# Kernel tuning notes

Measured on AMD Instinct MI355X. Metric: run time of the kernel, lower is better.

The kernel has to match this reference:

```python
import jax, jax.numpy as jnp
import numpy as np

N, E, G = 50000, 1600000, 64
N_SPECIES, D_ATTR, D, N_RBF = 16, 16, 32, 8
CUTOFF = 5.0
SCALE, SHIFT = 1.0, 0.0


def setup_inputs() -> dict:
    key = jax.random.key(0)
    ks = jax.random.split(key, 20)

    def w(k, shape):
        fan_in = shape[-2] if len(shape) > 1 else shape[-1]
        return jax.random.normal(k, shape, dtype=jnp.float32) / np.sqrt(fan_in)

    return {
        "x": jax.random.randint(ks[0], (N, 1), 0, N_SPECIES),
        "pos": 3.0 * jax.random.normal(ks[1], (N, 3), dtype=jnp.float32),
        "edge_index": jax.random.randint(ks[2], (2, E), 0, N),
        "period_vec": 0.1 * jax.random.normal(ks[3], (E, 3), dtype=jnp.float32),
        "batch": jnp.sort(jax.random.randint(ks[4], (N,), 0, G)),
        "W_elem": w(ks[5], (N_SPECIES, D_ATTR)),
        "W0": w(ks[6], (D_ATTR, D)),
        "b0": jnp.zeros((D,), jnp.float32),
        "Wr1": w(ks[7], (3, N_RBF, D)),
        "br1": jnp.zeros((3, D), jnp.float32),
        "Wr2": w(ks[8], (3, D, D)),
        "Wmsg": w(ks[9], (3, D, D)),
        "Wattr": w(ks[10], (3, D_ATTR, D)),
        "Wself": w(ks[11], (3, D, D)),
        "bconv": jnp.zeros((3, D), jnp.float32),
        "wsh": w(ks[12], (3, 4)),
        "Wp1": w(ks[13], (D, 16)),
        "bp1": jnp.zeros((16,), jnp.float32),
        "Wp2": w(ks[14], (16, 1)),
        "bp2": jnp.zeros((1,), jnp.float32),
    }


def reference(x, pos, edge_index, period_vec, batch, W_elem, W0, b0, Wr1, br1,
              Wr2, Wmsg, Wattr, Wself, bconv, wsh, Wp1, bp1, Wp2, bp2):
    src, dst = edge_index[0], edge_index[1]

    # node_attr_layer: species embedding (gather), then first_atom_embed linear
    x_attr = W_elem[x[:, 0]]                              # [N, D_ATTR]
    h = x_attr @ W0 + b0                                  # [N, D]

    # edge_attr_layer: PBC edge vectors, lengths, l<=1 spherical harmonics
    edge_vec = pos[dst] - pos[src] + period_vec           # [E, 3]
    edge_len = jnp.linalg.norm(edge_vec, axis=-1, keepdims=True)  # [E, 1]
    unit = edge_vec / (edge_len + 1e-9)
    edge_sh = jnp.concatenate([jnp.ones_like(edge_len), unit], axis=-1)  # [E, 4]

    # edge_embedding_layer: Gaussian radial basis of edge lengths
    centers = jnp.linspace(0.0, CUTOFF, N_RBF, dtype=pos.dtype)
    gamma = jnp.asarray((N_RBF / CUTOFF) ** 2, pos.dtype)
    rbf = jnp.exp(-gamma * (edge_len - centers) ** 2)     # [E, N_RBF]

    # 3 conv layers: gather -> per-edge transform -> scatter-sum -> node update
    for i in range(3):
        rw = jax.nn.relu(rbf @ Wr1[i] + br1[i]) @ Wr2[i]  # [E, D] radial MLP
        sh_w = edge_sh @ wsh[i]                           # [E] sh mixing
        msg = (h[src] @ Wmsg[i]) * rw * sh_w[:, None]     # [E, D]
        agg = jax.ops.segment_sum(msg, dst, num_segments=N)  # [N, D]
        h = jax.nn.silu(agg + x_attr @ Wattr[i] + h @ Wself[i] + bconv[i])

    # post_conv layers
    h = jax.nn.silu(h @ Wp1 + bp1)                        # [N, 16]
    h = (h @ Wp2 + bp2)[:, 0]                             # [N] (squeeze)

    # scatter-sum pooling over graphs + affine energy scaling
    e = jax.ops.segment_sum(h, batch, num_segments=G)     # [G]
    return (e * SCALE + SHIFT)[:, None]                   # [G, 1]
```

## Files before the change

### kernel.cpp

```cpp
#include <hip/hip_runtime.h>
#include <hip/hip_fp16.h>
#include <math.h>

constexpr int N_NODES  = 50000;
constexpr int N_EDGES  = 1600000;
constexpr int G_GRAPHS = 64;
constexpr int D        = 32;
constexpr int D_ATTR   = 16;
constexpr int N_RBF    = 8;

constexpr int   TBL      = 8192;
constexpr int   TBL_ROWS = TBL + 1;
constexpr float LMAX     = 10.0f;

constexpr int BUCKET = 80;

constexpr int NT     = 64;
constexpr int NTILES = (N_NODES + NT - 1) / NT;
constexpr int TCAP   = 2432;
constexpr int EPB      = 2048;
constexpr int STHREADS = 512;
constexpr int EPV      = EPB / STHREADS;
constexpr int NBLK1    = (N_EDGES + EPB - 1) / EPB;

constexpr int NSLOT = NTILES * NT * BUCKET;

typedef unsigned int  uint4v  __attribute__((ext_vector_type(4)));
typedef unsigned int  uint2v  __attribute__((ext_vector_type(2)));

__device__ __forceinline__ float silu(float x) {
    return x / (1.0f + __expf(-x));
}
__device__ __forceinline__ float h2f_bits(unsigned short u) {
    return __half2float(__ushort_as_half(u));
}
__device__ __forceinline__ __half2 h2u(unsigned v) {
    union { unsigned u; __half2 h; } c; c.u = v; return c.h;
}

__global__ void node_init_kernel(const int* __restrict__ x,
                                 const float* __restrict__ W_elem,
                                 const float* __restrict__ W0,
                                 const float* __restrict__ b0,
                                 const float* __restrict__ Wmsg0,
                                 const float* __restrict__ Wself0,
                                 const float* __restrict__ Wattr,
                                 const float* __restrict__ bconv,
                                 __half* __restrict__ hm0,
                                 float* __restrict__ hs0,
                                 float* __restrict__ xa1,
                                 float* __restrict__ xa2,
                                 float* __restrict__ out) {
    int t = blockIdx.x * blockDim.x + threadIdx.x;
    if (t < G_GRAPHS) out[t] = 0.0f;
    int n = t >> 5, c = t & 31;
    if (n >= N_NODES) return;
    int sp = x[n];
    const float* we = W_elem + sp * D_ATTR;
    float xv = (c < D_ATTR) ? we[c] : 0.0f;
    float acc = b0[c];
#pragma unroll
    for (int a = 0; a < D_ATTR; ++a) acc += we[a] * W0[a * D + c];
    float m = 0.0f, s = 0.0f;
#pragma unroll
    for (int j = 0; j < D; ++j) {
        float hj = __shfl(acc, j, 32);
        m = fmaf(hj, Wmsg0[j * D + c], m);
        s = fmaf(hj, Wself0[j * D + c], s);
    }
    float a0 = bconv[0 * D + c], a1 = bconv[1 * D + c], a2 = bconv[2 * D + c];
#pragma unroll
    for (int j = 0; j < D_ATTR; ++j) {
        float xj = __shfl(xv, j, 32);
        a0 = fmaf(xj, Wattr[0 * D_ATTR * D + j * D + c], a0);
        a1 = fmaf(xj, Wattr[1 * D_ATTR * D + j * D + c], a1);
        a2 = fmaf(xj, Wattr[2 * D_ATTR * D + j * D + c], a2);
    }
    hm0[n * D + c] = __float2half(m);
    hs0[n * D + c] = s + a0;
    xa1[n * D + c] = a1;
    xa2[n * D + c] = a2;
}

__global__ __launch_bounds__(STHREADS) void hist_kernel(const int* __restrict__ eidx,
                                                        int* __restrict__ blk_hist) {
    __shared__ int hist[NTILES];
    int tid = threadIdx.x;
    int e0 = blockIdx.x * EPB;
    for (int i = tid; i < NTILES; i += STHREADS) hist[i] = 0;
    __syncthreads();
#pragma unroll
    for (int i = 0; i < EPV; ++i) {
        int e = e0 + tid + STHREADS * i;
        if (e < N_EDGES) atomicAdd(&hist[eidx[N_EDGES + e] >> 6], 1);
    }
    __syncthreads();
    int* dst = blk_hist + (size_t)blockIdx.x * NTILES;
    for (int t = tid; t < NTILES; t += STHREADS) dst[t] = hist[t];
}

__global__ void scan_kernel(const int* __restrict__ blk_hist,
                            int* __restrict__ blk_base,
                            int* __restrict__ tile_total) {
    int t = blockIdx.x;
    int lane = threadIdx.x;
    int run = 0;
    for (int b0 = 0; b0 < NBLK1; b0 += 64) {
        int b = b0 + lane;
        int v = (b < NBLK1) ? blk_hist[(size_t)b * NTILES + t] : 0;
        int pre = v;
#pragma unroll
        for (int o = 1; o < 64; o <<= 1) {
            int w = __shfl_up(pre, o);
            if (lane >= o) pre += w;
        }
        int excl = pre - v;
        if (b < NBLK1) blk_base[(size_t)b * NTILES + t] = run + excl;
        run += __shfl(pre, 63);
    }
    if (lane == 0) tile_total[t] = run;
}

__global__ __launch_bounds__(STHREADS) void scatter_kernel(const int* __restrict__ eidx,
                                                           const float* __restrict__ pos,
                                                           const float* __restrict__ period,
                                                           const float* __restrict__ wsh,
                                                           const int* __restrict__ blk_base,
                                                           uint4v* __restrict__ bins) {
    __shared__ int hist[NTILES];
    __shared__ int basev[NTILES];
    int tid = threadIdx.x;
    int e0 = blockIdx.x * EPB;
    const int* bb = blk_base + (size_t)blockIdx.x * NTILES;
    for (int i = tid; i < NTILES; i += STHREADS) {
        hist[i] = 0;
        basev[i] = bb[i];
    }
    __syncthreads();

    int   sarr[EPV], darr[EPV];
    float vx[EPV], vy[EPV], vz[EPV];
#pragma unroll
    for (int i = 0; i < EPV; ++i) {
        int e  = e0 + tid + STHREADS * i;
        int ec = (e < N_EDGES) ? e : (N_EDGES - 1);
        int s = eidx[ec];
        int d = eidx[N_EDGES + ec];
        sarr[i] = s;
        darr[i] = d;
        vx[i] = pos[d * 3 + 0] - pos[s * 3 + 0] + period[ec * 3 + 0];
        vy[i] = pos[d * 3 + 1] - pos[s * 3 + 1] + period[ec * 3 + 1];
        vz[i] = pos[d * 3 + 2] - pos[s * 3 + 2] + period[ec * 3 + 2];
    }
    asm volatile("" ::
        "v"(vx[0]), "v"(vx[1]), "v"(vx[2]), "v"(vx[3]),
        "v"(vy[0]), "v"(vy[1]), "v"(vy[2]), "v"(vy[3]),
        "v"(vz[0]), "v"(vz[1]), "v"(vz[2]), "v"(vz[3]),
        "v"(sarr[0]), "v"(sarr[1]), "v"(sarr[2]), "v"(sarr[3]),
        "v"(darr[0]), "v"(darr[1]), "v"(darr[2]), "v"(darr[3]));
#pragma unroll
    for (int i = 0; i < EPV; ++i) {
        int e = e0 + tid + STHREADS * i;
        if (e >= N_EDGES) continue;
        float len = sqrtf(vx[i] * vx[i] + vy[i] * vy[i] + vz[i] * vz[i]);
        float inv = 1.0f / (len + 1e-9f);
        int idx = (int)fminf(len * ((float)TBL / LMAX) + 0.5f, (float)TBL);
        float sw[3];
#pragma unroll
        for (int l = 0; l < 3; ++l)
            sw[l] = wsh[l * 4 + 0] +
                    (vx[i] * wsh[l * 4 + 1] + vy[i] * wsh[l * 4 + 2] + vz[i] * wsh[l * 4 + 3]) * inv;
        int tile = darr[i] >> 6;
        int rank = atomicAdd(&hist[tile], 1);
        int slot = basev[tile] + rank;
        if (slot < TCAP) {
            unsigned u0 = (unsigned)__half_as_ushort(__float2half(sw[0]));
            unsigned u1 = (unsigned)__half_as_ushort(__float2half(sw[1]));
            unsigned u2 = (unsigned)__half_as_ushort(__float2half(sw[2]));
            uint4v r;
            r.x = (unsigned)sarr[i] | ((unsigned)idx << 16);
            r.y = (unsigned)(darr[i] & (NT - 1));
            r.z = u0 | (u1 << 16);
            r.w = u2;
            bins[(size_t)tile * TCAP + slot] = r;
        }
    }
}

__global__ __launch_bounds__(512) void shuffle_kernel(const uint4v* __restrict__ bins,
                                                      const int* __restrict__ tile_total,
                                                      unsigned int* __restrict__ xs,
                                                      unsigned short* __restrict__ swp,
                                                      int* __restrict__ count) {
    __shared__ int lcur[NT];
    int tile = blockIdx.x;
    int tid = threadIdx.x;
    if (tid < NT) lcur[tid] = 0;
    __syncthreads();
    int cnt = tile_total[tile];
    if (cnt > TCAP) cnt = TCAP;
    const uint4v* base = bins + (size_t)tile * TCAP;
    for (int i = tid; i < cnt; i += 512) {
        uint4v r = __builtin_nontemporal_load(base + i);
        int dl = (int)(r.y & 63u);
        int slot = atomicAdd(&lcur[dl], 1);
        if (slot < BUCKET) {
            size_t g = (size_t)(tile * NT + dl) * BUCKET + slot;
            xs[g] = r.x;
            swp[0 * (size_t)NSLOT + g] = (unsigned short)(r.z & 0xFFFFu);
            swp[1 * (size_t)NSLOT + g] = (unsigned short)(r.z >> 16);
            swp[2 * (size_t)NSLOT + g] = (unsigned short)(r.w & 0xFFFFu);
        }
    }
    __syncthreads();
    if (tid < NT) {
        int node = tile * NT + tid;
        if (node < N_NODES) {
            int c = lcur[tid];
            count[node] = c < BUCKET ? c : BUCKET;
        }
    }
}

__global__ void table_kernel(const float* __restrict__ Wr1,
                             const float* __restrict__ br1,
                             const float* __restrict__ Wr2,
                             __half* __restrict__ table) {
    int t = blockIdx.x * blockDim.x + threadIdx.x;
    if (t >= 3 * TBL_ROWS) return;
    int l = t / TBL_ROWS;
    int idx = t % TBL_ROWS;
    float len = (float)idx * (LMAX / (float)TBL);
    const float gamma = (8.0f / 5.0f) * (8.0f / 5.0f);
    float rbf[N_RBF];
#pragma unroll
    for (int k = 0; k < N_RBF; ++k) {
        float dd = len - (float)k * (5.0f / 7.0f);
        rbf[k] = __expf(-gamma * dd * dd);
    }
    float out[D];
#pragma unroll
    for (int c = 0; c < D; ++c) out[c] = 0.0f;
    for (int j = 0; j < D; ++j) {
        float z = br1[l * D + j];
#pragma unroll
        for (int k = 0; k < N_RBF; ++k) z += rbf[k] * Wr1[l * N_RBF * D + k * D + j];
        z = fmaxf(z, 0.0f);
        const float* w2 = Wr2 + l * D * D + j * D;
#pragma unroll
        for (int c = 0; c < D; ++c) out[c] += z * w2[c];
    }
    __half* dst = table + ((size_t)(l * TBL_ROWS + idx)) * D;
#pragma unroll
    for (int c = 0; c < D; ++c) dst[c] = __float2half(out[c]);
}

template <int LAYER, bool NEXT>
__global__ __launch_bounds__(256, 4) void conv_kernel(const __half* __restrict__ hm,
                            const float* __restrict__ hs,
                            const unsigned int* __restrict__ xs,
                            const unsigned short* __restrict__ swp,
                            const int* __restrict__ count,
                            const __half* __restrict__ table,
                            const float* __restrict__ Wmsg_next,
                            const float* __restrict__ Wself_next,
                            const float* __restrict__ xa_next,
                            __half* __restrict__ hm_out,
                            float* __restrict__ hs_out,
                            float* __restrict__ h_final) {
    int gtid = blockIdx.x * blockDim.x + threadIdx.x;
    int node = gtid >> 6;
    if (node >= N_NODES) return;
    int lane = threadIdx.x & 63;
    int qw = lane >> 4;
    int q  = lane & 15;

    const unsigned* tab2 = (const unsigned*)(table + ((size_t)LAYER * TBL_ROWS) * D);
    const unsigned* hm2  = (const unsigned*)hm;
    const unsigned short* swb = swp + (size_t)LAYER * NSLOT;
    int cnt = count[node];
    int beg = node * BUCKET;
    int end = beg + cnt;

    float ax = 0.0f, ay = 0.0f;
    for (int base = beg; base < end; base += 32) {
        int o0 = base + qw * 4;
        int o1 = o0 + 16;
        uint4v x0 = __builtin_nontemporal_load((const uint4v*)(xs + o0));
        uint4v x1 = __builtin_nontemporal_load((const uint4v*)(xs + o1));
        uint2v w0 = __builtin_nontemporal_load((const uint2v*)(swb + o0));
        uint2v w1 = __builtin_nontemporal_load((const uint2v*)(swb + o1));
        unsigned u[8];
        unsigned short wv[8];
        u[0] = x0.x; u[1] = x0.y; u[2] = x0.z; u[3] = x0.w;
        u[4] = x1.x; u[5] = x1.y; u[6] = x1.z; u[7] = x1.w;
        wv[0] = (unsigned short)(w0.x & 0xFFFFu); wv[1] = (unsigned short)(w0.x >> 16);
        wv[2] = (unsigned short)(w0.y & 0xFFFFu); wv[3] = (unsigned short)(w0.y >> 16);
        wv[4] = (unsigned short)(w1.x & 0xFFFFu); wv[5] = (unsigned short)(w1.x >> 16);
        wv[6] = (unsigned short)(w1.y & 0xFFFFu); wv[7] = (unsigned short)(w1.y >> 16);
        unsigned tvu[8], mvu[8];
#pragma unroll
        for (int j = 0; j < 8; ++j) {
            int slot = (j < 4) ? (o0 + j) : (o1 + j - 4);
            unsigned uu = (slot < end) ? u[j] : 0u;
            int s = (int)(uu & 0xFFFFu);
            int i = (int)(uu >> 16);
            tvu[j] = tab2[i * 16 + q];
            mvu[j] = hm2[s * 16 + q];
        }
        asm volatile("" ::
            "v"(tvu[0]), "v"(tvu[1]), "v"(tvu[2]), "v"(tvu[3]),
            "v"(tvu[4]), "v"(tvu[5]), "v"(tvu[6]), "v"(tvu[7]),
            "v"(mvu[0]), "v"(mvu[1]), "v"(mvu[2]), "v"(mvu[3]),
            "v"(mvu[4]), "v"(mvu[5]), "v"(mvu[6]), "v"(mvu[7]));
#pragma unroll
        for (int j = 0; j < 8; ++j) {
            int slot = (j < 4) ? (o0 + j) : (o1 + j - 4);
            float sw = (slot < end) ? h2f_bits(wv[j]) : 0.0f;
            __half2 p = __hmul2(h2u(tvu[j]), h2u(mvu[j]));
            float2 pf = __half22float2(p);
            ax = fmaf(pf.x, sw, ax);
            ay = fmaf(pf.y, sw, ay);
        }
    }
    ax += __shfl_xor(ax, 16);
    ax += __shfl_xor(ax, 32);
    ay += __shfl_xor(ay, 16);
    ay += __shfl_xor(ay, 32);

    int c = lane & 31;
    float vx = __shfl(ax, c >> 1);
    float vy = __shfl(ay, c >> 1);
    float agg = (c & 1) ? vy : vx;

    if ((lane >> 5) == 0) {
        float hn = silu(agg + hs[node * D + c]);
        if (NEXT) {
            float m = 0.0f, s2 = 0.0f;
#pragma unroll
            for (int j = 0; j < D; ++j) {
                float hj = __shfl(hn, j);
                m  = fmaf(hj, Wmsg_next[j * D + c], m);
                s2 = fmaf(hj, Wself_next[j * D + c], s2);
            }
            hm_out[node * D + c] = __float2half(m);
            hs_out[node * D + c] = s2 + xa_next[node * D + c];
        } else {
            h_final[node * D + c] = hn;
        }
    }
}

__global__ void readout_kernel(const float* __restrict__ h,
                               const int* __restrict__ batch,
                               const float* __restrict__ Wp1,
                               const float* __restrict__ bp1,
                               const float* __restrict__ Wp2,
                               const float* __restrict__ bp2,
                               float* __restrict__ out) {
    int n = blockIdx.x * blockDim.x + threadIdx.x;
    float s = 0.0f;
    int b = -1;
    if (n < N_NODES) {
        b = batch[n];
        const float* hrow = h + n * D;
        float acc2 = bp2[0];
#pragma unroll
        for (int m = 0; m < 16; ++m) {
            float a = bp1[m];
#pragma unroll
            for (int j = 0; j < D; ++j) a += hrow[j] * Wp1[j * 16 + m];
            acc2 += silu(a) * Wp2[m];
        }
        s = acc2;
    }
    unsigned long long valid = __ballot(n < N_NODES);
    if (valid == 0ull) return;
    int firstLane = __ffsll(valid) - 1;
    int b0v = __shfl(b, firstLane);
    bool ok = (b == b0v) || (n >= N_NODES);
    if (__all(ok)) {
#pragma unroll
        for (int o = 32; o > 0; o >>= 1) s += __shfl_down(s, o);
        if ((threadIdx.x & 63) == 0) atomicAdd(out + b0v, s);
    } else {
        if (n < N_NODES) atomicAdd(out + b, s);
    }
}

extern "C" void kernel_launch(void* const* d_in, const int* in_sizes, int n_in,
                              void* d_out, int out_size, void* d_ws, size_t ws_size,
                              hipStream_t stream) {
    const int*   x      = (const int*)d_in[0];
    const float* pos    = (const float*)d_in[1];
    const int*   eidx   = (const int*)d_in[2];
    const float* period = (const float*)d_in[3];
    const int*   batch  = (const int*)d_in[4];
    const float* W_elem = (const float*)d_in[5];
    const float* W0     = (const float*)d_in[6];
    const float* b0     = (const float*)d_in[7];
    const float* Wr1    = (const float*)d_in[8];
    const float* br1    = (const float*)d_in[9];
    const float* Wr2    = (const float*)d_in[10];
    const float* Wmsg   = (const float*)d_in[11];
    const float* Wattr  = (const float*)d_in[12];
    const float* Wself  = (const float*)d_in[13];
    const float* bconv  = (const float*)d_in[14];
    const float* wsh    = (const float*)d_in[15];
    const float* Wp1    = (const float*)d_in[16];
    const float* bp1    = (const float*)d_in[17];
    const float* Wp2    = (const float*)d_in[18];
    const float* bp2    = (const float*)d_in[19];

    char* base = (char*)d_ws;
    size_t off = 0;
    auto carve = [&](size_t bytes) -> void* {
        void* p = base + off;
        off = (off + bytes + 255) & ~(size_t)255;
        return p;
    };
    __half*         hm_a        = (__half*)carve((size_t)N_NODES * D * 2);
    __half*         hm_b        = (__half*)carve((size_t)N_NODES * D * 2);
    float*          hs_a        = (float*)carve((size_t)N_NODES * D * 4);
    float*          hs_b        = (float*)carve((size_t)N_NODES * D * 4);
    float*          xa1         = (float*)carve((size_t)N_NODES * D * 4);
    float*          xa2         = (float*)carve((size_t)N_NODES * D * 4);
    float*          h_final     = (float*)carve((size_t)N_NODES * D * 4);
    unsigned int*   xs          = (unsigned int*)carve((size_t)NSLOT * 4);
    unsigned short* swp         = (unsigned short*)carve((size_t)3 * NSLOT * 2);
    uint4v*         bins        = (uint4v*)carve((size_t)NTILES * TCAP * 16);
    int*            blk_hist    = (int*)carve((size_t)NBLK1 * NTILES * 4);
    int*            blk_base    = (int*)carve((size_t)NBLK1 * NTILES * 4);
    int*            tile_total  = (int*)carve((size_t)NTILES * 4);
    int*            count       = (int*)carve((size_t)NTILES * NT * 4);
    __half*         table       = (__half*)carve((size_t)3 * TBL_ROWS * D * 2);
    (void)ws_size; (void)in_sizes; (void)n_in; (void)out_size;

    node_init_kernel<<<(N_NODES * 32 + 255) / 256, 256, 0, stream>>>(
        x, W_elem, W0, b0, Wmsg + 0 * D * D, Wself + 0 * D * D, Wattr, bconv,
        hm_a, hs_a, xa1, xa2, (float*)d_out);
    hist_kernel<<<NBLK1, STHREADS, 0, stream>>>(eidx, blk_hist);
    scan_kernel<<<NTILES, 64, 0, stream>>>(blk_hist, blk_base, tile_total);
    scatter_kernel<<<NBLK1, STHREADS, 0, stream>>>(eidx, pos, period, wsh, blk_base, bins);
    table_kernel<<<(3 * TBL_ROWS + 127) / 128, 128, 0, stream>>>(Wr1, br1, Wr2, table);
    shuffle_kernel<<<NTILES, 512, 0, stream>>>(bins, tile_total, xs, swp, count);

    int cgrid = (N_NODES * 64 + 255) / 256;
    conv_kernel<0, true><<<cgrid, 256, 0, stream>>>(
        hm_a, hs_a, xs, swp, count, table, Wmsg + 1 * D * D, Wself + 1 * D * D, xa1,
        hm_b, hs_b, nullptr);
    conv_kernel<1, true><<<cgrid, 256, 0, stream>>>(
        hm_b, hs_b, xs, swp, count, table, Wmsg + 2 * D * D, Wself + 2 * D * D, xa2,
        hm_a, hs_a, nullptr);
    conv_kernel<2, false><<<cgrid, 256, 0, stream>>>(
        hm_a, hs_a, xs, swp, count, table, nullptr, nullptr, nullptr,
        nullptr, nullptr, h_final);

    readout_kernel<<<(N_NODES + 255) / 256, 256, 0, stream>>>(h_final, batch, Wp1, bp1, Wp2, bp2,
                                                              (float*)d_out);
}
```

Measured before the change: 401.6 us.

## Process two nodes per wavefront in conv kernel to double gather ILP

Each 64-lane wavefront in the conv kernel now handles two destination nodes instead of one. The bucket loops for both nodes are interleaved so twice as many independent table and feature gathers are in flight per iteration. The epilogue uses both half-waves, one per node, where before the upper half sat idle. Launch bounds rise to 5 waves per SIMD and the grid is halved. In exchange, register pressure goes up and the two nodes' loops run to the larger of their edge counts.

```diff
diff --git a/kernel.cpp b/kernel.cpp
--- a/kernel.cpp
+++ b/kernel.cpp
@@ -256,7 +256,7 @@
 }
 
 template <int LAYER, bool NEXT>
-__global__ __launch_bounds__(256, 4) void conv_kernel(const __half* __restrict__ hm,
+__global__ __launch_bounds__(256, 5) void conv_kernel(const __half* __restrict__ hm,
                             const float* __restrict__ hs,
                             const unsigned int* __restrict__ xs,
                             const unsigned short* __restrict__ swp,
@@ -268,9 +268,10 @@
                             __half* __restrict__ hm_out,
                             float* __restrict__ hs_out,
                             float* __restrict__ h_final) {
-    int gtid = blockIdx.x * blockDim.x + threadIdx.x;
-    int node = gtid >> 6;
-    if (node >= N_NODES) return;
+    int wid = (blockIdx.x * blockDim.x + threadIdx.x) >> 6;
+    int na = wid * 2;
+    if (na >= N_NODES) return;
+    int nb = na + 1;
     int lane = threadIdx.x & 63;
     int qw = lane >> 4;
     int q  = lane & 15;
@@ -278,76 +279,105 @@
     const unsigned* tab2 = (const unsigned*)(table + ((size_t)LAYER * TBL_ROWS) * D);
     const unsigned* hm2  = (const unsigned*)hm;
     const unsigned short* swb = swp + (size_t)LAYER * NSLOT;
-    int cnt = count[node];
-    int beg = node * BUCKET;
-    int end = beg + cnt;
-
-    float ax = 0.0f, ay = 0.0f;
-    for (int base = beg; base < end; base += 32) {
-        int o0 = base + qw * 4;
-        int o1 = o0 + 16;
-        uint4v x0 = __builtin_nontemporal_load((const uint4v*)(xs + o0));
-        uint4v x1 = __builtin_nontemporal_load((const uint4v*)(xs + o1));
-        uint2v w0 = __builtin_nontemporal_load((const uint2v*)(swb + o0));
-        uint2v w1 = __builtin_nontemporal_load((const uint2v*)(swb + o1));
-        unsigned u[8];
-        unsigned short wv[8];
-        u[0] = x0.x; u[1] = x0.y; u[2] = x0.z; u[3] = x0.w;
-        u[4] = x1.x; u[5] = x1.y; u[6] = x1.z; u[7] = x1.w;
-        wv[0] = (unsigned short)(w0.x & 0xFFFFu); wv[1] = (unsigned short)(w0.x >> 16);
-        wv[2] = (unsigned short)(w0.y & 0xFFFFu); wv[3] = (unsigned short)(w0.y >> 16);
-        wv[4] = (unsigned short)(w1.x & 0xFFFFu); wv[5] = (unsigned short)(w1.x >> 16);
-        wv[6] = (unsigned short)(w1.y & 0xFFFFu); wv[7] = (unsigned short)(w1.y >> 16);
-        unsigned tvu[8], mvu[8];
+
+    int cnta = count[na], cntb = count[nb];
+    int bega = na * BUCKET, begb = nb * BUCKET;
+    int enda = bega + cnta, endb = begb + cntb;
+    int mx = cnta > cntb ? cnta : cntb;
+
+    float axa = 0.0f, aya = 0.0f, axb = 0.0f, ayb = 0.0f;
+    for (int k = 0; k < BUCKET; k += 32) {
+        int o0a = bega + k + qw * 4, o1a = o0a + 16;
+        int o0b = begb + k + qw * 4, o1b = o0b + 16;
+        uint4v xa0 = __builtin_nontemporal_load((const uint4v*)(xs + o0a));
+        uint4v xa1 = __builtin_nontemporal_load((const uint4v*)(xs + o1a));
+        uint4v xb0 = __builtin_nontemporal_load((const uint4v*)(xs + o0b));
+        uint4v xb1 = __builtin_nontemporal_load((const uint4v*)(xs + o1b));
+        uint2v wa0 = __builtin_nontemporal_load((const uint2v*)(swb + o0a));
+        uint2v wa1 = __builtin_nontemporal_load((const uint2v*)(swb + o1a));
+        uint2v wb0 = __builtin_nontemporal_load((const uint2v*)(swb + o0b));
+        uint2v wb1 = __builtin_nontemporal_load((const uint2v*)(swb + o1b));
+        unsigned ua[8] = {xa0.x, xa0.y, xa0.z, xa0.w, xa1.x, xa1.y, xa1.z, xa1.w};
+        unsigned ub[8] = {xb0.x, xb0.y, xb0.z, xb0.w, xb1.x, xb1.y, xb1.z, xb1.w};
+        unsigned tva[8], mva[8], tvb[8], mvb[8];
 #pragma unroll
         for (int j = 0; j < 8; ++j) {
-            int slot = (j < 4) ? (o0 + j) : (o1 + j - 4);
-            unsigned uu = (slot < end) ? u[j] : 0u;
-            int s = (int)(uu & 0xFFFFu);
-            int i = (int)(uu >> 16);
-            tvu[j] = tab2[i * 16 + q];
-            mvu[j] = hm2[s * 16 + q];
+            int slot = (j < 4) ? (o0a + j) : (o1a + j - 4);
+            unsigned uu = (slot < enda) ? ua[j] : 0u;
+            tva[j] = tab2[(int)(uu >> 16) * 16 + q];
+            mva[j] = hm2[(int)(uu & 0xFFFFu) * 16 + q];
+        }
+#pragma unroll
+        for (int j = 0; j < 8; ++j) {
+            int slot = (j < 4) ? (o0b + j) : (o1b + j - 4);
+            unsigned uu = (slot < endb) ? ub[j] : 0u;
+            tvb[j] = tab2[(int)(uu >> 16) * 16 + q];
+            mvb[j] = hm2[(int)(uu & 0xFFFFu) * 16 + q];
         }
         asm volatile("" ::
-            "v"(tvu[0]), "v"(tvu[1]), "v"(tvu[2]), "v"(tvu[3]),
-            "v"(tvu[4]), "v"(tvu[5]), "v"(tvu[6]), "v"(tvu[7]),
-            "v"(mvu[0]), "v"(mvu[1]), "v"(mvu[2]), "v"(mvu[3]),
-            "v"(mvu[4]), "v"(mvu[5]), "v"(mvu[6]), "v"(mvu[7]));
+            "v"(tva[0]), "v"(tva[1]), "v"(tva[2]), "v"(tva[3]),
+            "v"(tva[4]), "v"(tva[5]), "v"(tva[6]), "v"(tva[7]),
+            "v"(mva[0]), "v"(mva[1]), "v"(mva[2]), "v"(mva[3]),
+            "v"(mva[4]), "v"(mva[5]), "v"(mva[6]), "v"(mva[7]),
+            "v"(tvb[0]), "v"(tvb[1]), "v"(tvb[2]), "v"(tvb[3]),
+            "v"(tvb[4]), "v"(tvb[5]), "v"(tvb[6]), "v"(tvb[7]),
+            "v"(mvb[0]), "v"(mvb[1]), "v"(mvb[2]), "v"(mvb[3]),
+            "v"(mvb[4]), "v"(mvb[5]), "v"(mvb[6]), "v"(mvb[7]));
+        unsigned short wva[8] = {
+            (unsigned short)(wa0.x & 0xFFFFu), (unsigned short)(wa0.x >> 16),
+            (unsigned short)(wa0.y & 0xFFFFu), (unsigned short)(wa0.y >> 16),
+            (unsigned short)(wa1.x & 0xFFFFu), (unsigned short)(wa1.x >> 16),
+            (unsigned short)(wa1.y & 0xFFFFu), (unsigned short)(wa1.y >> 16)};
+        unsigned short wvb[8] = {
+            (unsigned short)(wb0.x & 0xFFFFu), (unsigned short)(wb0.x >> 16),
+            (unsigned short)(wb0.y & 0xFFFFu), (unsigned short)(wb0.y >> 16),
+            (unsigned short)(wb1.x & 0xFFFFu), (unsigned short)(wb1.x >> 16),
+            (unsigned short)(wb1.y & 0xFFFFu), (unsigned short)(wb1.y >> 16)};
 #pragma unroll
         for (int j = 0; j < 8; ++j) {
-            int slot = (j < 4) ? (o0 + j) : (o1 + j - 4);
-            float sw = (slot < end) ? h2f_bits(wv[j]) : 0.0f;
-            __half2 p = __hmul2(h2u(tvu[j]), h2u(mvu[j]));
-            float2 pf = __half22float2(p);
-            ax = fmaf(pf.x, sw, ax);
-            ay = fmaf(pf.y, sw, ay);
-        }
-    }
-    ax += __shfl_xor(ax, 16);
-    ax += __shfl_xor(ax, 32);
-    ay += __shfl_xor(ay, 16);
-    ay += __shfl_xor(ay, 32);
+            int slot = (j < 4) ? (o0a + j) : (o1a + j - 4);
+            float sw = (slot < enda) ? h2f_bits(wva[j]) : 0.0f;
+            float2 pf = __half22float2(__hmul2(h2u(tva[j]), h2u(mva[j])));
+            axa = fmaf(pf.x, sw, axa);
+            aya = fmaf(pf.y, sw, aya);
+        }
+#pragma unroll
+        for (int j = 0; j < 8; ++j) {
+            int slot = (j < 4) ? (o0b + j) : (o1b + j - 4);
+            float sw = (slot < endb) ? h2f_bits(wvb[j]) : 0.0f;
+            float2 pf = __half22float2(__hmul2(h2u(tvb[j]), h2u(mvb[j])));
+            axb = fmaf(pf.x, sw, axb);
+            ayb = fmaf(pf.y, sw, ayb);
+        }
+        if (k + 32 >= mx) break;
+    }
+    axa += __shfl_xor(axa, 16); axa += __shfl_xor(axa, 32);
+    aya += __shfl_xor(aya, 16); aya += __shfl_xor(aya, 32);
+    axb += __shfl_xor(axb, 16); axb += __shfl_xor(axb, 32);
+    ayb += __shfl_xor(ayb, 16); ayb += __shfl_xor(ayb, 32);
 
     int c = lane & 31;
-    float vx = __shfl(ax, c >> 1);
-    float vy = __shfl(ay, c >> 1);
-    float agg = (c & 1) ? vy : vx;
-
-    if ((lane >> 5) == 0) {
-        float hn = silu(agg + hs[node * D + c]);
-        if (NEXT) {
-            float m = 0.0f, s2 = 0.0f;
-#pragma unroll
-            for (int j = 0; j < D; ++j) {
-                float hj = __shfl(hn, j);
-                m  = fmaf(hj, Wmsg_next[j * D + c], m);
-                s2 = fmaf(hj, Wself_next[j * D + c], s2);
-            }
-            hm_out[node * D + c] = __float2half(m);
-            hs_out[node * D + c] = s2 + xa_next[node * D + c];
-        } else {
-            h_final[node * D + c] = hn;
-        }
+    float vxa = __shfl(axa, c >> 1), vya = __shfl(aya, c >> 1);
+    float vxb = __shfl(axb, c >> 1), vyb = __shfl(ayb, c >> 1);
+    float agga = (c & 1) ? vya : vxa;
+    float aggb = (c & 1) ? vyb : vxb;
+    bool hi = lane >= 32;
+    int mynode = hi ? nb : na;
+    float agg = hi ? aggb : agga;
+
+    float hn = silu(agg + hs[mynode * D + c]);
+    if (NEXT) {
+        float m = 0.0f, s2 = 0.0f;
+#pragma unroll
+        for (int j = 0; j < D; ++j) {
+            float hj = __shfl(hn, j, 32);
+            m  = fmaf(hj, Wmsg_next[j * D + c], m);
+            s2 = fmaf(hj, Wself_next[j * D + c], s2);
+        }
+        hm_out[mynode * D + c] = __float2half(m);
+        hs_out[mynode * D + c] = s2 + xa_next[mynode * D + c];
+    } else {
+        h_final[mynode * D + c] = hn;
     }
 }
 
@@ -445,7 +475,8 @@
     table_kernel<<<(3 * TBL_ROWS + 127) / 128, 128, 0, stream>>>(Wr1, br1, Wr2, table);
     shuffle_kernel<<<NTILES, 512, 0, stream>>>(bins, tile_total, xs, swp, count);
 
-    int cgrid = (N_NODES * 64 + 255) / 256;
+    int cwaves = (N_NODES + 1) / 2;
+    int cgrid  = (cwaves * 64 + 255) / 256;
     conv_kernel<0, true><<<cgrid, 256, 0, stream>>>(
         hm_a, hs_a, xs, swp, count, table, Wmsg + 1 * D * D, Wself + 1 * D * D, xa1,
         hm_b, hs_b, nullptr);
```

Measured after the change: 388.8 us. 1.03x faster.

## Drop per-node shuffle; aggregate tile bins directly via LDS atomics in conv

Applied to the files above, without the earlier changes.

Removes the shuffle kernel that regrouped tile bins into fixed-size per-node buckets. Each conv kernel now processes one 64-node tile per 512-thread block, reads the 16-byte bin records directly, gathers table and feature rows with 16-byte vector loads, and accumulates messages into a shared-memory array with float atomics. This saves one kernel launch, the xs/swp/count buffers and their traffic, and also drops the per-node 80-edge cap. In exchange it adds LDS atomic contention, reads the full 16-byte bin records in every layer, and has fewer blocks (NTILES) with a different occupancy profile.

```diff
diff --git a/kernel.cpp b/kernel.cpp
--- a/kernel.cpp
+++ b/kernel.cpp
@@ -12,8 +12,6 @@
 constexpr int   TBL      = 8192;
 constexpr int   TBL_ROWS = TBL + 1;
 constexpr float LMAX     = 10.0f;
-
-constexpr int BUCKET = 80;
 
 constexpr int NT     = 64;
 constexpr int NTILES = (N_NODES + NT - 1) / NT;
@@ -22,8 +20,6 @@
 constexpr int STHREADS = 512;
 constexpr int EPV      = EPB / STHREADS;
 constexpr int NBLK1    = (N_EDGES + EPB - 1) / EPB;
-
-constexpr int NSLOT = NTILES * NT * BUCKET;
 
 typedef unsigned int  uint4v  __attribute__((ext_vector_type(4)));
 typedef unsigned int  uint2v  __attribute__((ext_vector_type(2)));
@@ -187,41 +183,6 @@
     }
 }
 
-__global__ __launch_bounds__(512) void shuffle_kernel(const uint4v* __restrict__ bins,
-                                                      const int* __restrict__ tile_total,
-                                                      unsigned int* __restrict__ xs,
-                                                      unsigned short* __restrict__ swp,
-                                                      int* __restrict__ count) {
-    __shared__ int lcur[NT];
-    int tile = blockIdx.x;
-    int tid = threadIdx.x;
-    if (tid < NT) lcur[tid] = 0;
-    __syncthreads();
-    int cnt = tile_total[tile];
-    if (cnt > TCAP) cnt = TCAP;
-    const uint4v* base = bins + (size_t)tile * TCAP;
-    for (int i = tid; i < cnt; i += 512) {
-        uint4v r = __builtin_nontemporal_load(base + i);
-        int dl = (int)(r.y & 63u);
-        int slot = atomicAdd(&lcur[dl], 1);
-        if (slot < BUCKET) {
-            size_t g = (size_t)(tile * NT + dl) * BUCKET + slot;
-            xs[g] = r.x;
-            swp[0 * (size_t)NSLOT + g] = (unsigned short)(r.z & 0xFFFFu);
-            swp[1 * (size_t)NSLOT + g] = (unsigned short)(r.z >> 16);
-            swp[2 * (size_t)NSLOT + g] = (unsigned short)(r.w & 0xFFFFu);
-        }
-    }
-    __syncthreads();
-    if (tid < NT) {
-        int node = tile * NT + tid;
-        if (node < N_NODES) {
-            int c = lcur[tid];
-            count[node] = c < BUCKET ? c : BUCKET;
-        }
-    }
-}
-
 __global__ void table_kernel(const float* __restrict__ Wr1,
                              const float* __restrict__ br1,
                              const float* __restrict__ Wr2,
@@ -256,11 +217,10 @@
 }
 
 template <int LAYER, bool NEXT>
-__global__ __launch_bounds__(256, 4) void conv_kernel(const __half* __restrict__ hm,
+__global__ __launch_bounds__(512) void conv_kernel(const __half* __restrict__ hm,
                             const float* __restrict__ hs,
-                            const unsigned int* __restrict__ xs,
-                            const unsigned short* __restrict__ swp,
-                            const int* __restrict__ count,
+                            const uint4v* __restrict__ bins,
+                            const int* __restrict__ tile_total,
                             const __half* __restrict__ table,
                             const float* __restrict__ Wmsg_next,
                             const float* __restrict__ Wself_next,
@@ -268,85 +228,72 @@
                             __half* __restrict__ hm_out,
                             float* __restrict__ hs_out,
                             float* __restrict__ h_final) {
-    int gtid = blockIdx.x * blockDim.x + threadIdx.x;
-    int node = gtid >> 6;
-    if (node >= N_NODES) return;
-    int lane = threadIdx.x & 63;
-    int qw = lane >> 4;
-    int q  = lane & 15;
-
-    const unsigned* tab2 = (const unsigned*)(table + ((size_t)LAYER * TBL_ROWS) * D);
-    const unsigned* hm2  = (const unsigned*)hm;
-    const unsigned short* swb = swp + (size_t)LAYER * NSLOT;
-    int cnt = count[node];
-    int beg = node * BUCKET;
-    int end = beg + cnt;
-
-    float ax = 0.0f, ay = 0.0f;
-    for (int base = beg; base < end; base += 32) {
-        int o0 = base + qw * 4;
-        int o1 = o0 + 16;
-        uint4v x0 = __builtin_nontemporal_load((const uint4v*)(xs + o0));
-        uint4v x1 = __builtin_nontemporal_load((const uint4v*)(xs + o1));
-        uint2v w0 = __builtin_nontemporal_load((const uint2v*)(swb + o0));
-        uint2v w1 = __builtin_nontemporal_load((const uint2v*)(swb + o1));
-        unsigned u[8];
-        unsigned short wv[8];
-        u[0] = x0.x; u[1] = x0.y; u[2] = x0.z; u[3] = x0.w;
-        u[4] = x1.x; u[5] = x1.y; u[6] = x1.z; u[7] = x1.w;
-        wv[0] = (unsigned short)(w0.x & 0xFFFFu); wv[1] = (unsigned short)(w0.x >> 16);
-        wv[2] = (unsigned short)(w0.y & 0xFFFFu); wv[3] = (unsigned short)(w0.y >> 16);
-        wv[4] = (unsigned short)(w1.x & 0xFFFFu); wv[5] = (unsigned short)(w1.x >> 16);
-        wv[6] = (unsigned short)(w1.y & 0xFFFFu); wv[7] = (unsigned short)(w1.y >> 16);
-        unsigned tvu[8], mvu[8];
-#pragma unroll
-        for (int j = 0; j < 8; ++j) {
-            int slot = (j < 4) ? (o0 + j) : (o1 + j - 4);
-            unsigned uu = (slot < end) ? u[j] : 0u;
-            int s = (int)(uu & 0xFFFFu);
-            int i = (int)(uu >> 16);
-            tvu[j] = tab2[i * 16 + q];
-            mvu[j] = hm2[s * 16 + q];
-        }
-        asm volatile("" ::
-            "v"(tvu[0]), "v"(tvu[1]), "v"(tvu[2]), "v"(tvu[3]),
-            "v"(tvu[4]), "v"(tvu[5]), "v"(tvu[6]), "v"(tvu[7]),
-            "v"(mvu[0]), "v"(mvu[1]), "v"(mvu[2]), "v"(mvu[3]),
-            "v"(mvu[4]), "v"(mvu[5]), "v"(mvu[6]), "v"(mvu[7]));
-#pragma unroll
-        for (int j = 0; j < 8; ++j) {
-            int slot = (j < 4) ? (o0 + j) : (o1 + j - 4);
-            float sw = (slot < end) ? h2f_bits(wv[j]) : 0.0f;
-            __half2 p = __hmul2(h2u(tvu[j]), h2u(mvu[j]));
-            float2 pf = __half22float2(p);
-            ax = fmaf(pf.x, sw, ax);
-            ay = fmaf(pf.y, sw, ay);
-        }
-    }
-    ax += __shfl_xor(ax, 16);
-    ax += __shfl_xor(ax, 32);
-    ay += __shfl_xor(ay, 16);
-    ay += __shfl_xor(ay, 32);
-
-    int c = lane & 31;
-    float vx = __shfl(ax, c >> 1);
-    float vy = __shfl(ay, c >> 1);
-    float agg = (c & 1) ? vy : vx;
-
-    if ((lane >> 5) == 0) {
-        float hn = silu(agg + hs[node * D + c]);
-        if (NEXT) {
-            float m = 0.0f, s2 = 0.0f;
-#pragma unroll
-            for (int j = 0; j < D; ++j) {
-                float hj = __shfl(hn, j);
-                m  = fmaf(hj, Wmsg_next[j * D + c], m);
-                s2 = fmaf(hj, Wself_next[j * D + c], s2);
+    __shared__ float acc[NT][D + 1];
+    int tile = blockIdx.x;
+    int tid  = threadIdx.x;
+    for (int i = tid; i < NT * (D + 1); i += 512) (&acc[0][0])[i] = 0.0f;
+    __syncthreads();
+
+    int cnt = tile_total[tile];
+    if (cnt > TCAP) cnt = TCAP;
+    const uint4v* base = bins + (size_t)tile * TCAP;
+    const uint4v* tab4 = (const uint4v*)(table + (size_t)LAYER * TBL_ROWS * D);
+    const uint4v* hm4  = (const uint4v*)hm;
+    int lane = tid & 63;
+    int rg = lane >> 2;
+    int cg = lane & 3;
+    int wv = tid >> 6;
+
+    for (int i0 = wv * 16; i0 < cnt; i0 += 128) {
+        int i = i0 + rg;
+        bool v = i < cnt;
+        int ic = v ? i : cnt - 1;
+        uint4v r = base[ic];
+        unsigned sx = r.x;
+        int dl = (int)(r.y & 63u);
+        unsigned short swu = (LAYER == 0) ? (unsigned short)(r.z & 0xFFFFu)
+                           : (LAYER == 1) ? (unsigned short)(r.z >> 16)
+                                          : (unsigned short)(r.w & 0xFFFFu);
+        float sw = v ? h2f_bits(swu) : 0.0f;
+        uint4v t = tab4[(size_t)(sx >> 16) * 4 + cg];
+        uint4v m = hm4[(size_t)(sx & 0xFFFFu) * 4 + cg];
+        float2 p0 = __half22float2(__hmul2(h2u(t.x), h2u(m.x)));
+        float2 p1 = __half22float2(__hmul2(h2u(t.y), h2u(m.y)));
+        float2 p2 = __half22float2(__hmul2(h2u(t.z), h2u(m.z)));
+        float2 p3 = __half22float2(__hmul2(h2u(t.w), h2u(m.w)));
+        float* a = &acc[dl][cg * 8];
+        atomicAdd(a + 0, p0.x * sw);
+        atomicAdd(a + 1, p0.y * sw);
+        atomicAdd(a + 2, p1.x * sw);
+        atomicAdd(a + 3, p1.y * sw);
+        atomicAdd(a + 4, p2.x * sw);
+        atomicAdd(a + 5, p2.y * sw);
+        atomicAdd(a + 6, p3.x * sw);
+        atomicAdd(a + 7, p3.y * sw);
+    }
+    __syncthreads();
+
+    int grp = tid >> 5;
+    int c   = tid & 31;
+#pragma unroll
+    for (int rr = 0; rr < 4; ++rr) {
+        int nl = rr * 16 + grp;
+        int node = tile * NT + nl;
+        if (node < N_NODES) {
+            float hn = silu(acc[nl][c] + hs[node * D + c]);
+            if (NEXT) {
+                float m = 0.0f, s2 = 0.0f;
+#pragma unroll
+                for (int j = 0; j < D; ++j) {
+                    float hj = __shfl(hn, j, 32);
+                    m  = fmaf(hj, Wmsg_next[j * D + c], m);
+                    s2 = fmaf(hj, Wself_next[j * D + c], s2);
+                }
+                hm_out[node * D + c] = __float2half(m);
+                hs_out[node * D + c] = s2 + xa_next[node * D + c];
+            } else {
+                h_final[node * D + c] = hn;
             }
-            hm_out[node * D + c] = __float2half(m);
-            hs_out[node * D + c] = s2 + xa_next[node * D + c];
-        } else {
-            h_final[node * D + c] = hn;
         }
     }
 }
@@ -426,13 +373,10 @@
     float*          xa1         = (float*)carve((size_t)N_NODES * D * 4);
     float*          xa2         = (float*)carve((size_t)N_NODES * D * 4);
     float*          h_final     = (float*)carve((size_t)N_NODES * D * 4);
-    unsigned int*   xs          = (unsigned int*)carve((size_t)NSLOT * 4);
-    unsigned short* swp         = (unsigned short*)carve((size_t)3 * NSLOT * 2);
     uint4v*         bins        = (uint4v*)carve((size_t)NTILES * TCAP * 16);
     int*            blk_hist    = (int*)carve((size_t)NBLK1 * NTILES * 4);
     int*            blk_base    = (int*)carve((size_t)NBLK1 * NTILES * 4);
     int*            tile_total  = (int*)carve((size_t)NTILES * 4);
-    int*            count       = (int*)carve((size_t)NTILES * NT * 4);
     __half*         table       = (__half*)carve((size_t)3 * TBL_ROWS * D * 2);
     (void)ws_size; (void)in_sizes; (void)n_in; (void)out_size;
 
@@ -443,17 +387,15 @@
     scan_kernel<<<NTILES, 64, 0, stream>>>(blk_hist, blk_base, tile_total);
     scatter_kernel<<<NBLK1, STHREADS, 0, stream>>>(eidx, pos, period, wsh, blk_base, bins);
     table_kernel<<<(3 * TBL_ROWS + 127) / 128, 128, 0, stream>>>(Wr1, br1, Wr2, table);
-    shuffle_kernel<<<NTILES, 512, 0, stream>>>(bins, tile_total, xs, swp, count);
-
-    int cgrid = (N_NODES * 64 + 255) / 256;
-    conv_kernel<0, true><<<cgrid, 256, 0, stream>>>(
-        hm_a, hs_a, xs, swp, count, table, Wmsg + 1 * D * D, Wself + 1 * D * D, xa1,
+
+    conv_kernel<0, true><<<NTILES, 512, 0, stream>>>(
+        hm_a, hs_a, bins, tile_total, table, Wmsg + 1 * D * D, Wself + 1 * D * D, xa1,
         hm_b, hs_b, nullptr);
-    conv_kernel<1, true><<<cgrid, 256, 0, stream>>>(
-        hm_b, hs_b, xs, swp, count, table, Wmsg + 2 * D * D, Wself + 2 * D * D, xa2,
+    conv_kernel<1, true><<<NTILES, 512, 0, stream>>>(
+        hm_b, hs_b, bins, tile_total, table, Wmsg + 2 * D * D, Wself + 2 * D * D, xa2,
         hm_a, hs_a, nullptr);
-    conv_kernel<2, false><<<cgrid, 256, 0, stream>>>(
-        hm_a, hs_a, xs, swp, count, table, nullptr, nullptr, nullptr,
+    conv_kernel<2, false><<<NTILES, 512, 0, stream>>>(
+        hm_a, hs_a, bins, tile_total, table, nullptr, nullptr, nullptr,
         nullptr, nullptr, h_final);
 
     readout_kernel<<<(N_NODES + 255) / 256, 256, 0, stream>>>(h_final, batch, Wp1, bp1, Wp2, bp2,
```

After: 1.285 ms. +219.8%, slower.
